# Kernel tuning notes

Measured on AMD Instinct MI355X. Metric: run time of the kernel, lower is better.

## Reference

```python
import jax, jax.numpy as jnp
import numpy as np

B, G, GS = 1024, 2000, 25   # batch, num gene groups, group size
H1, H2, C = 1024, 512, 10
EPS = 1e-5


def _xavier(key, shape, fan_in, fan_out):
    lim = np.sqrt(6.0 / (fan_in + fan_out))
    return jax.random.uniform(key, shape, jnp.float32, -lim, lim)


def setup_inputs() -> dict:
    key = jax.random.key(0)
    ks = jax.random.split(key, 8)
    x = jax.random.normal(ks[0], (B, G * GS), jnp.float32)
    # per-group Linear(GS, 1) weights stacked -> block-diagonal grouped GEMM
    gene_w = _xavier(ks[1], (G, GS), GS, 1)
    gene_b = jnp.zeros((G,), jnp.float32)
    W1 = _xavier(ks[2], (G, H1), G, H1)
    b1 = jnp.zeros((H1,), jnp.float32)
    W2 = _xavier(ks[3], (H1, H2), H1, H2)
    b2 = jnp.zeros((H2,), jnp.float32)
    Wout = _xavier(ks[4], (H2, C), H2, C)
    bout = jnp.zeros((C,), jnp.float32)
    Wres = _xavier(ks[5], (G, C), G, C)
    bres = jnp.zeros((C,), jnp.float32)
    gamma1 = jnp.ones((H1,), jnp.float32); beta1 = jnp.zeros((H1,), jnp.float32)
    gamma2 = jnp.ones((H2,), jnp.float32); beta2 = jnp.zeros((H2,), jnp.float32)
    return dict(x=x, gene_w=gene_w, gene_b=gene_b, W1=W1, b1=b1,
                gamma1=gamma1, beta1=beta1, W2=W2, b2=b2,
                gamma2=gamma2, beta2=beta2, Wout=Wout, bout=bout,
                Wres=Wres, bres=bres)


def _batch_norm(h, gamma, beta):
    # training-mode BatchNorm1d: biased batch statistics over axis 0
    mu = jnp.mean(h, axis=0)
    var = jnp.mean(jnp.square(h - mu), axis=0)
    return gamma * (h - mu) * jax.lax.rsqrt(var + EPS) + beta


def reference(x, gene_w, gene_b, W1, b1, gamma1, beta1, W2, b2,
              gamma2, beta2, Wout, bout, Wres, bres):
    # fused replacement for the per-group Linear(GS,1)+ReLU loop + cat
    xg = x.reshape(B, G, GS)
    g = jax.nn.relu(jnp.einsum('bgk,gk->bg', xg, gene_w) + gene_b)  # [B, G]
    h1 = jax.nn.relu(_batch_norm(g @ W1 + b1, gamma1, beta1))       # [B, H1]
    h2 = jax.nn.relu(_batch_norm(h1 @ W2 + b2, gamma2, beta2))      # [B, H2]
    x_main = h2 @ Wout + bout                                       # [B, C]
    x_res = g @ Wres + bres                                         # [B, C]
    return jax.nn.softmax(x_main + x_res, axis=1)
```

## Files before the change

### kernel.cpp

```cpp
#include <hip/hip_runtime.h>
#include <math.h>

#define NB   1024
#define NG   2000
#define NGS  25
#define KP   2048
#define NH1  1024
#define NH1X 1088
#define NH2  512
#define NC   10
#define EPSV 1e-5f
#define GPB  200
#define RB   8


typedef __attribute__((ext_vector_type(8)))  __bf16 bf16x8;
typedef __attribute__((ext_vector_type(4)))  float  f32x4;
typedef __attribute__((ext_vector_type(16))) float  f32x16;
typedef __attribute__((ext_vector_type(8)))  unsigned short u16x8;

__device__ __forceinline__ unsigned short f2bf(float f) {
  union { float f; unsigned u; } v; v.f = f;
  return (unsigned short)((v.u + 0x7fffu + ((v.u >> 16) & 1u)) >> 16);
}

__global__ __launch_bounds__(256) void prep_kernel(
    const float* __restrict__ x, const float* __restrict__ gw,
    const float* __restrict__ gb, unsigned short* __restrict__ g_bf,
    const float* __restrict__ W1, unsigned short* __restrict__ W1bT,
    const float* __restrict__ W2, unsigned short* __restrict__ W2bT,
    const float* __restrict__ Wres, float* __restrict__ stats) {
  __shared__ __attribute__((aligned(16))) float xs[2][GPB * NGS];
  int t = threadIdx.x;

  if (blockIdx.y < 10) {
    int blk = blockIdx.y;
    int b0 = blockIdx.x * RB;
    const size_t chunk_off = (size_t)blk * (GPB * NGS);

    float4 st[5];
#pragma unroll
    for (int j = 0; j < 5; ++j) st[j] = make_float4(0.f, 0.f, 0.f, 0.f);
    {
      const float4* s0 = (const float4*)(x + (size_t)b0 * (NG * NGS) + chunk_off);
#pragma unroll
      for (int j = 0; j < 5; ++j) {
        int i = t + j * 256;
        if (i < (GPB * NGS) / 4) st[j] = s0[i];
      }
    }
    const float4* gsrc = (const float4*)(gw + chunk_off);
    float4* xd0 = (float4*)xs[0];
    for (int i = t; i < (GPB * NGS) / 4; i += 256) xd0[i] = gsrc[i];
    __syncthreads();
    float gwr[NGS];
    float gbv = 0.f;
    int gi = blk * GPB + t;
    if (t < GPB) {
#pragma unroll
      for (int k = 0; k < NGS; ++k) gwr[k] = xs[0][t * NGS + k];
      gbv = gb[gi];
    }
    __syncthreads();

    for (int r = 0; r < RB; ++r) {
      float* xc = xs[r & 1];
      float4* xdc = (float4*)xc;
#pragma unroll
      for (int j = 0; j < 5; ++j) {
        int i = t + j * 256;
        if (i < (GPB * NGS) / 4) xdc[i] = st[j];
      }
      __syncthreads();
      if (r + 1 < RB) {
        const float4* sn = (const float4*)
            (x + (size_t)(b0 + r + 1) * (NG * NGS) + chunk_off);
#pragma unroll
        for (int j = 0; j < 5; ++j) {
          int i = t + j * 256;
          if (i < (GPB * NGS) / 4) st[j] = sn[i];
        }
      }
      int b = b0 + r;
      if (t < GPB) {
        float acc = 0.f;
        const float* xp = xc + t * NGS;
#pragma unroll
        for (int k = 0; k < NGS; ++k) acc = fmaf(xp[k], gwr[k], acc);
        g_bf[(size_t)b * KP + gi] = f2bf(fmaxf(acc + gbv, 0.f));
      } else if (blk == 9 && t < GPB + (KP - NG)) {
        g_bf[(size_t)b * KP + NG + (t - GPB)] = 0;
      }
    }
    return;
  }

  int px = (blockIdx.y - 10) * 128 + blockIdx.x;
  if (px == 672) {
    for (int i = t; i < 3072; i += 256) stats[i] = 0.f;
    return;
  }
  if (px > 672) return;
  const float* src; unsigned short* dst; int K, N, Kpad, k0, n0;
  int wres_mode = 0;
  if (px < 512)      { src = W1; dst = W1bT; K = NG;  N = NH1; Kpad = KP;
                       k0 = (px & 31) * 64; n0 = (px >> 5) * 64; }
  else if (px < 640) { int xi = px - 512;
                       src = W2; dst = W2bT; K = NH1; N = NH2; Kpad = NH1;
                       k0 = (xi & 15) * 64; n0 = (xi >> 4) * 64; }
  else               { int xi = px - 640;
                       src = Wres; dst = W1bT; K = NG; N = NC; Kpad = KP;
                       k0 = xi * 64; n0 = 1024; wres_mode = 1; }

  unsigned short (*ts)[72] = (unsigned short (*)[72])xs;
  int c4 = (t & 15) * 4;
  int r  = t >> 4;
  for (int rr = r; rr < 64; rr += 16) {
    int k = k0 + rr;
    float v[4] = {0.f, 0.f, 0.f, 0.f};
    if (!wres_mode) {
      if (k < K) {
        float4 q = *(const float4*)&src[(size_t)k * N + n0 + c4];
        v[0] = q.x; v[1] = q.y; v[2] = q.z; v[3] = q.w;
      }
    } else {
      if (k < K) {
#pragma unroll
        for (int i = 0; i < 4; ++i)
          if (c4 + i < NC) v[i] = src[(size_t)k * NC + c4 + i];
      }
    }
    ts[rr][c4 + 0] = f2bf(v[0]); ts[rr][c4 + 1] = f2bf(v[1]);
    ts[rr][c4 + 2] = f2bf(v[2]); ts[rr][c4 + 3] = f2bf(v[3]);
  }
  __syncthreads();
  int rr8 = (t & 7) * 8;
  int cc  = t >> 3;
  for (int c = cc; c < 64; c += 32) {
    u16x8 val;
#pragma unroll
    for (int i = 0; i < 8; ++i) val[i] = ts[rr8 + i][c];
    *(u16x8*)&dst[(size_t)(n0 + c) * Kpad + k0 + rr8] = val;
  }
}

__global__ __launch_bounds__(256) void gemm1_kernel(
    const unsigned short* __restrict__ A,
    const unsigned short* __restrict__ Bt,
    float* __restrict__ C, float* __restrict__ sum, float* __restrict__ sq,
    float* __restrict__ rpx, int M, int N, int Kp) {
  __shared__ unsigned short As[32][68];
  __shared__ unsigned short Bs[64][68];
  __shared__ float ebuf[2 * 64 * 17];
  int t = threadIdx.x;
  int m0 = blockIdx.y * 32, n0 = blockIdx.x * 64;
  int wave = t >> 6, lane = t & 63;
  int h = wave & 1;
  int p = wave >> 1;
  int l31 = lane & 31, l5 = lane >> 5;
  int srow = t >> 3, skc = (t & 7) * 8;

  f32x16 acc;
#pragma unroll
  for (int q = 0; q < 16; ++q) acc[q] = 0.f;

  const unsigned short* Ap = A + (size_t)(m0 + srow) * Kp + skc;
  const unsigned short* Bp = Bt + (size_t)(n0 + srow) * Kp + skc;
  size_t rstep = 32 * (size_t)Kp;

  u16x8 pa0 = *(const u16x8*)(Ap);
  u16x8 pb0 = *(const u16x8*)(Bp);
  u16x8 pb1 = *(const u16x8*)(Bp + rstep);

  for (int k0 = 0; k0 < Kp; k0 += 64) {
    *(u16x8*)&As[srow][skc]      = pa0;
    *(u16x8*)&Bs[srow][skc]      = pb0;
    *(u16x8*)&Bs[srow + 32][skc] = pb1;
    __syncthreads();
    if (k0 + 64 < Kp) {
      pa0 = *(const u16x8*)(Ap + k0 + 64);
      pb0 = *(const u16x8*)(Bp + k0 + 64);
      pb1 = *(const u16x8*)(Bp + k0 + 64 + rstep);
    }
    int kb = p * 32 + l5 * 8;
    {
      bf16x8 av = *(const bf16x8*)&As[l31][kb];
      bf16x8 bv = *(const bf16x8*)&Bs[h * 32 + l31][kb];
      acc = __builtin_amdgcn_mfma_f32_32x32x16_bf16(av, bv, acc, 0, 0, 0);
    }
    {
      bf16x8 av = *(const bf16x8*)&As[l31][kb + 16];
      bf16x8 bv = *(const bf16x8*)&Bs[h * 32 + l31][kb + 16];
      acc = __builtin_amdgcn_mfma_f32_32x32x16_bf16(av, bv, acc, 0, 0, 0);
    }
    __syncthreads();
  }

  float* eb = ebuf + (size_t)(h * 64 + lane) * 17;
  if (p == 1) {
#pragma unroll
    for (int r = 0; r < 16; ++r) eb[r] = acc[r];
  }
  __syncthreads();
  if (p == 0) {
    float s = 0.f, ss = 0.f;
#pragma unroll
    for (int r = 0; r < 16; ++r) {
      float v = acc[r] + eb[r];
      int row = m0 + (r & 3) + 8 * (r >> 2) + 4 * l5;
      if (n0 < N) {
        C[(size_t)row * N + n0 + h * 32 + l31] = v;
        s += v;
        ss = fmaf(v, v, ss);
      } else {
        rpx[(size_t)row * 64 + h * 32 + l31] = v;
      }
    }
    if (n0 < N) {
      s  += __shfl_down(s, 32, 64);
      ss += __shfl_down(ss, 32, 64);
      if (lane < 32) {
        atomicAdd(&sum[n0 + h * 32 + lane], s);
        atomicAdd(&sq[n0 + h * 32 + lane], ss);
      }
    }
  }
}

__global__ __launch_bounds__(256) void gemm2_kernel(
    const float* __restrict__ A,
    const unsigned short* __restrict__ Bt,
    float* __restrict__ C, const float* __restrict__ sum1,
    const float* __restrict__ sq1, const float* __restrict__ gam1,
    const float* __restrict__ bet1, float* __restrict__ sum2,
    float* __restrict__ sq2, int M, int N, int Kp) {
  __shared__ unsigned short As[32][72];
  __shared__ unsigned short Bs[32][72];
  __shared__ float sc1s[NH1], sh1s[NH1];
  int t = threadIdx.x;
  int m0 = blockIdx.y * 32, n0 = blockIdx.x * 32;
  int wave = t >> 6, lane = t & 63;
  int wm = (wave >> 1) * 16, wn = (wave & 1) * 16;
  int fm = lane & 15, fk = (lane >> 4) * 8;
  int srow = t >> 3, skc = (t & 7) * 8;

  for (int k = t; k < Kp; k += 256) {
    float mu  = sum1[k] * (1.f / NB);
    float var = sq1[k] * (1.f / NB) - mu * mu;
    float scv = gam1[k] * rsqrtf(var + EPSV);
    sc1s[k] = scv;
    sh1s[k] = fmaf(-mu, scv, bet1[k]);
  }

  f32x4 acc = (f32x4){0.f, 0.f, 0.f, 0.f};

  const float* Ap = A + (size_t)(m0 + srow) * Kp + skc;
  const unsigned short* Bp = Bt + (size_t)(n0 + srow) * Kp + skc;

  f32x4 pa0 = *(const f32x4*)(Ap);
  f32x4 pa1 = *(const f32x4*)(Ap + 4);
  u16x8 pb0 = *(const u16x8*)(Bp);
  __syncthreads();

  for (int k0 = 0; k0 < Kp; k0 += 64) {
    f32x4 scl = *(const f32x4*)&sc1s[k0 + skc];
    f32x4 sch = *(const f32x4*)&sc1s[k0 + skc + 4];
    f32x4 shl = *(const f32x4*)&sh1s[k0 + skc];
    f32x4 shh = *(const f32x4*)&sh1s[k0 + skc + 4];
    u16x8 a0;
#pragma unroll
    for (int i = 0; i < 4; ++i) {
      a0[i]     = f2bf(fmaxf(fmaf(pa0[i], scl[i], shl[i]), 0.f));
      a0[i + 4] = f2bf(fmaxf(fmaf(pa1[i], sch[i], shh[i]), 0.f));
    }
    *(u16x8*)&As[srow][skc] = a0;
    *(u16x8*)&Bs[srow][skc] = pb0;
    __syncthreads();
    if (k0 + 64 < Kp) {
      pa0 = *(const f32x4*)(Ap + k0 + 64);
      pa1 = *(const f32x4*)(Ap + k0 + 64 + 4);
      pb0 = *(const u16x8*)(Bp + k0 + 64);
    }
#pragma unroll
    for (int s = 0; s < 2; ++s) {
      bf16x8 af = *(const bf16x8*)&As[wm + fm][s * 32 + fk];
      bf16x8 bf = *(const bf16x8*)&Bs[wn + fm][s * 32 + fk];
      acc = __builtin_amdgcn_mfma_f32_16x16x32_bf16(af, bf, acc, 0, 0, 0);
    }
    __syncthreads();
  }

  int crow = (lane >> 4) * 4, ccol = lane & 15;
  float s = 0.f, ss = 0.f;
#pragma unroll
  for (int r = 0; r < 4; ++r) {
    float v = acc[r];
    int m = m0 + wm + crow + r;
    int n = n0 + wn + ccol;
    C[(size_t)m * N + n] = v;
    s += v;
    ss = fmaf(v, v, ss);
  }
  s  += __shfl_down(s, 32, 64);  s  += __shfl_down(s, 16, 64);
  ss += __shfl_down(ss, 32, 64); ss += __shfl_down(ss, 16, 64);
  if (lane < 16) {
    atomicAdd(&sum2[n0 + wn + lane], s);
    atomicAdd(&sq2[n0 + wn + lane], ss);
  }
}

__global__ __launch_bounds__(256) void final_kernel(
    const float* __restrict__ t2, const float* __restrict__ sum2,
    const float* __restrict__ sq2, const float* __restrict__ gam2,
    const float* __restrict__ bet2, const float* __restrict__ rpx,
    const float* __restrict__ Wout, const float* __restrict__ bout,
    const float* __restrict__ bres, float* __restrict__ out) {
  __shared__ __attribute__((aligned(16))) float wl[NH2 * NC];
  __shared__ float red[4][NC];
  __shared__ float logits[NC];
  int b = blockIdx.x;
  int t = threadIdx.x;

  const float4* wsrc = (const float4*)Wout;
  float4* wdst = (float4*)wl;
#pragma unroll
  for (int i = 0; i < (NH2 * NC / 4) / 256; ++i)
    wdst[t + i * 256] = wsrc[t + i * 256];
  __syncthreads();

  float acc[NC] = {};
#pragma unroll
  for (int half = 0; half < 2; ++half) {
    int h = t + half * 256;
    float raw = t2[(size_t)b * NH2 + h];
    float mu  = sum2[h] * (1.f / NB);
    float var = sq2[h] * (1.f / NB) - mu * mu;
    float scv = gam2[h] * rsqrtf(var + EPSV);
    float hr  = fmaxf(fmaf(raw, scv, fmaf(-mu, scv, bet2[h])), 0.f);
    const float* wrow = &wl[h * NC];
#pragma unroll
    for (int c = 0; c < NC; ++c) acc[c] = fmaf(hr, wrow[c], acc[c]);
  }

  int lane = t & 63, wave = t >> 6;
#pragma unroll
  for (int c = 0; c < NC; ++c) {
    float v = acc[c];
    for (int off = 32; off > 0; off >>= 1) v += __shfl_down(v, off, 64);
    if (lane == 0) red[wave][c] = v;
  }
  __syncthreads();
  if (t < NC) {
    logits[t] = red[0][t] + red[1][t] + red[2][t] + red[3][t] +
                bout[t] + bres[t] + rpx[(size_t)b * 64 + t];
  }
  __syncthreads();
  if (t == 0) {
    float mx = logits[0];
#pragma unroll
    for (int c = 1; c < NC; ++c) mx = fmaxf(mx, logits[c]);
    float e[NC], s = 0.f;
#pragma unroll
    for (int c = 0; c < NC; ++c) { e[c] = expf(logits[c] - mx); s += e[c]; }
    float inv = 1.f / s;
#pragma unroll
    for (int c = 0; c < NC; ++c) out[(size_t)b * NC + c] = e[c] * inv;
  }
}

extern "C" void kernel_launch(void* const* d_in, const int* in_sizes, int n_in,
                              void* d_out, int out_size, void* d_ws, size_t ws_size,
                              hipStream_t stream) {
  const float* x      = (const float*)d_in[0];
  const float* gw     = (const float*)d_in[1];
  const float* gb     = (const float*)d_in[2];
  const float* W1     = (const float*)d_in[3];
  const float* gamma1 = (const float*)d_in[5];
  const float* beta1  = (const float*)d_in[6];
  const float* W2     = (const float*)d_in[7];
  const float* gamma2 = (const float*)d_in[9];
  const float* beta2  = (const float*)d_in[10];
  const float* Wout   = (const float*)d_in[11];
  const float* bout   = (const float*)d_in[12];
  const float* Wres   = (const float*)d_in[13];
  const float* bres   = (const float*)d_in[14];
  float* out = (float*)d_out;

  char* p = (char*)d_ws;
  unsigned short* g_bf = (unsigned short*)p; p += (size_t)NB * KP * 2;
  unsigned short* W1bT = (unsigned short*)p; p += (size_t)NH1X * KP * 2;
  unsigned short* W2bT = (unsigned short*)p; p += (size_t)NH2 * NH1 * 2;
  float* t1 = (float*)p; p += (size_t)NB * NH1 * 4;
  float* t2 = (float*)p; p += (size_t)NB * NH2 * 4;
  float* stats = (float*)p; p += 3072 * 4;
  float* rpx = (float*)p; p += (size_t)NB * 64 * 4;
  float* sum1 = stats, *sq1 = stats + 1024, *sum2 = stats + 2048, *sq2 = stats + 2560;

  prep_kernel<<<dim3(128, 16), 256, 0, stream>>>(x, gw, gb, g_bf,
                                                 W1, W1bT, W2, W2bT,
                                                 Wres, stats);

  gemm1_kernel<<<dim3(NH1X / 64, NB / 32), 256, 0, stream>>>(
      g_bf, W1bT, t1, sum1, sq1, rpx, NB, NH1, KP);

  gemm2_kernel<<<dim3(NH2 / 32, NB / 32), 256, 0, stream>>>(
      t1, W2bT, t2, sum1, sq1, gamma1, beta1, sum2, sq2, NB, NH2, NH1);

  final_kernel<<<NB, 256, 0, stream>>>(t2, sum2, sq2, gamma2, beta2, rpx,
                                       Wout, bout, bres, out);
}
```

Baseline: 359.8 us.

## Split gene-dot prep into per-wave smem slices to drop block barriers

Restructures the grouped gene dot-product stage so each of the four waves owns a 50-group slice of the 200-group chunk in its own shared-memory region. Each wave loads its slice with a 2-float alignment offset. Because no wave reads another wave's data, the __syncthreads barriers inside the row loop go away. The loop also double-buffers row loads in registers (stA/stB) so the next row's global load overlaps the current dot product. In exchange it uses more registers and relies on wave-synchronous ordering of LDS writes and reads within a wave.

Result: no change. 355.5 us (-1.2%).

```diff
diff --git a/kernel.cpp b/kernel.cpp
--- a/kernel.cpp
+++ b/kernel.cpp
@@ -30,67 +30,86 @@
     const float* __restrict__ W1, unsigned short* __restrict__ W1bT,
     const float* __restrict__ W2, unsigned short* __restrict__ W2bT,
     const float* __restrict__ Wres, float* __restrict__ stats) {
-  __shared__ __attribute__((aligned(16))) float xs[2][GPB * NGS];
+  __shared__ __attribute__((aligned(16))) float xsl[4][1284];
   int t = threadIdx.x;
 
   if (blockIdx.y < 10) {
     int blk = blockIdx.y;
     int b0 = blockIdx.x * RB;
-    const size_t chunk_off = (size_t)blk * (GPB * NGS);
-
-    float4 st[5];
-#pragma unroll
-    for (int j = 0; j < 5; ++j) st[j] = make_float4(0.f, 0.f, 0.f, 0.f);
+    int w = t >> 6, l = t & 63;
+    int d = (w & 1) * 2;
+    size_t wchunk = (size_t)blk * (GPB * NGS) + w * 1250 - d;
+    float4* slice4 = (float4*)xsl[w];
+    const float* xrd = xsl[w] + d;
+
+    float4 sg[5], stA[5], stB[5];
+    const float4* gw4 = (const float4*)gw + (wchunk >> 2);
+#pragma unroll
+    for (int j = 0; j < 5; ++j) {
+      int idx = l + j * 64;
+      sg[j] = (idx < 313) ? gw4[idx] : make_float4(0.f, 0.f, 0.f, 0.f);
+    }
     {
-      const float4* s0 = (const float4*)(x + (size_t)b0 * (NG * NGS) + chunk_off);
+      const float4* x0 = (const float4*)x + (((size_t)b0 * (NG * NGS) + wchunk) >> 2);
 #pragma unroll
       for (int j = 0; j < 5; ++j) {
-        int i = t + j * 256;
-        if (i < (GPB * NGS) / 4) st[j] = s0[i];
-      }
-    }
-    const float4* gsrc = (const float4*)(gw + chunk_off);
-    float4* xd0 = (float4*)xs[0];
-    for (int i = t; i < (GPB * NGS) / 4; i += 256) xd0[i] = gsrc[i];
-    __syncthreads();
+        int idx = l + j * 64;
+        stA[j] = (idx < 313) ? x0[idx] : make_float4(0.f, 0.f, 0.f, 0.f);
+      }
+    }
+#pragma unroll
+    for (int j = 0; j < 5; ++j) {
+      int idx = l + j * 64;
+      if (idx < 313) slice4[idx] = sg[j];
+    }
     float gwr[NGS];
     float gbv = 0.f;
-    int gi = blk * GPB + t;
-    if (t < GPB) {
-#pragma unroll
-      for (int k = 0; k < NGS; ++k) gwr[k] = xs[0][t * NGS + k];
-      gbv = gb[gi];
-    }
-    __syncthreads();
-
-    for (int r = 0; r < RB; ++r) {
-      float* xc = xs[r & 1];
-      float4* xdc = (float4*)xc;
+    if (l < 50) {
+#pragma unroll
+      for (int k = 0; k < NGS; ++k) gwr[k] = xrd[l * 25 + k];
+      gbv = gb[blk * GPB + w * 50 + l];
+    }
+
+    auto publish = [&](const float4* st) {
 #pragma unroll
       for (int j = 0; j < 5; ++j) {
-        int i = t + j * 256;
-        if (i < (GPB * NGS) / 4) xdc[i] = st[j];
-      }
-      __syncthreads();
-      if (r + 1 < RB) {
-        const float4* sn = (const float4*)
-            (x + (size_t)(b0 + r + 1) * (NG * NGS) + chunk_off);
-#pragma unroll
-        for (int j = 0; j < 5; ++j) {
-          int i = t + j * 256;
-          if (i < (GPB * NGS) / 4) st[j] = sn[i];
+        int idx = l + j * 64;
+        if (idx < 313) slice4[idx] = st[j];
+      }
+    };
+    auto issue = [&](float4* st, int row) {
+      const float4* xn = (const float4*)x + (((size_t)row * (NG * NGS) + wchunk) >> 2);
+#pragma unroll
+      for (int j = 0; j < 5; ++j) {
+        int idx = l + j * 64;
+        st[j] = (idx < 313) ? xn[idx] : make_float4(0.f, 0.f, 0.f, 0.f);
+      }
+    };
+    auto dot = [&](int b) {
+      if (l < 50) {
+        float acc = 0.f;
+#pragma unroll
+        for (int k = 0; k < NGS; ++k) acc = fmaf(xrd[l * 25 + k], gwr[k], acc);
+        g_bf[(size_t)b * KP + blk * GPB + w * 50 + l] =
+            f2bf(fmaxf(acc + gbv, 0.f));
+      } else if (blk == 9 && w == 0) {
+#pragma unroll
+        for (int j = 0; j < 4; ++j) {
+          int pp = (l - 50) + 14 * j;
+          if (pp < KP - NG) g_bf[(size_t)b * KP + NG + pp] = 0;
         }
       }
-      int b = b0 + r;
-      if (t < GPB) {
-        float acc = 0.f;
-        const float* xp = xc + t * NGS;
-#pragma unroll
-        for (int k = 0; k < NGS; ++k) acc = fmaf(xp[k], gwr[k], acc);
-        g_bf[(size_t)b * KP + gi] = f2bf(fmaxf(acc + gbv, 0.f));
-      } else if (blk == 9 && t < GPB + (KP - NG)) {
-        g_bf[(size_t)b * KP + NG + (t - GPB)] = 0;
-      }
+    };
+
+#pragma unroll
+    for (int rr = 0; rr < RB / 2; ++rr) {
+      int rA = rr * 2;
+      publish(stA);
+      issue(stB, b0 + rA + 1);
+      dot(b0 + rA);
+      publish(stB);
+      if (rA + 2 < RB) issue(stA, b0 + rA + 2);
+      dot(b0 + rA + 1);
     }
     return;
   }
@@ -112,7 +131,7 @@
                        src = Wres; dst = W1bT; K = NG; N = NC; Kpad = KP;
                        k0 = xi * 64; n0 = 1024; wres_mode = 1; }
 
-  unsigned short (*ts)[72] = (unsigned short (*)[72])xs;
+  unsigned short (*ts)[72] = (unsigned short (*)[72])xsl;
   int c4 = (t & 15) * 4;
   int r  = t >> 4;
   for (int rr = r; rr < 64; rr += 16) {
```

## Compute grouped gene projection with block-diagonal bf16 MFMA GEMM tiles

Applied to the files above, without the earlier changes.

Replaces the scalar per-group dot-product stage with a tiled MFMA formulation. Each block takes 32 batch rows and 64 groups and builds a block-diagonal bf16 weight tile in shared memory. It streams x converted to bf16 and accumulates with 32x32x16 MFMA, with a split-K reduction across wave pairs. The aim is to make the memory-bound x read more efficient through wider, better-distributed tiles and a larger grid. In exchange it wastes most MFMA work on zeros and rounds x to bf16 before the reduction, which lowers accuracy.

Result: no change. 362.4 us (+0.7%).

```diff
diff --git a/kernel.cpp b/kernel.cpp
--- a/kernel.cpp
+++ b/kernel.cpp
@@ -4,14 +4,13 @@
 #define NB   1024
 #define NG   2000
 #define NGS  25
+#define XW   (NG * NGS)
 #define KP   2048
 #define NH1  1024
 #define NH1X 1088
 #define NH2  512
 #define NC   10
 #define EPSV 1e-5f
-#define GPB  200
-#define RB   8
 
 
 typedef __attribute__((ext_vector_type(8)))  __bf16 bf16x8;
@@ -30,72 +29,99 @@
     const float* __restrict__ W1, unsigned short* __restrict__ W1bT,
     const float* __restrict__ W2, unsigned short* __restrict__ W2bT,
     const float* __restrict__ Wres, float* __restrict__ stats) {
-  __shared__ __attribute__((aligned(16))) float xs[2][GPB * NGS];
+  __shared__ __attribute__((aligned(16))) char smem[34816];
   int t = threadIdx.x;
 
-  if (blockIdx.y < 10) {
-    int blk = blockIdx.y;
-    int b0 = blockIdx.x * RB;
-    const size_t chunk_off = (size_t)blk * (GPB * NGS);
-
-    float4 st[5];
-#pragma unroll
-    for (int j = 0; j < 5; ++j) st[j] = make_float4(0.f, 0.f, 0.f, 0.f);
+  if (blockIdx.y < 32) {
+    unsigned short (*As)[68] = (unsigned short (*)[68])smem;
+    unsigned short (*Bs)[68] = (unsigned short (*)[68])(smem + 8704);
+    float* ebuf = (float*)(smem + 8704 + 17408);
+    int g0 = blockIdx.x * 64;
+    int m0 = blockIdx.y * 32;
+    int wave = t >> 6, lane = t & 63;
+    int h = wave & 1, p = wave >> 1;
+    int l31 = lane & 31, l5 = lane >> 5;
+    int srow = t >> 3, skc = (t & 7) * 8;
+
+    f32x16 acc;
+#pragma unroll
+    for (int q = 0; q < 16; ++q) acc[q] = 0.f;
+
+    const float* xrow = x + (size_t)(m0 + srow) * XW;
+    const int cbase = g0 * NGS + skc;
+    const float* gwb = gw + (size_t)g0 * NGS;
+
+    float4 pa0 = make_float4(0.f, 0.f, 0.f, 0.f), pa1 = pa0;
     {
-      const float4* s0 = (const float4*)(x + (size_t)b0 * (NG * NGS) + chunk_off);
-#pragma unroll
-      for (int j = 0; j < 5; ++j) {
-        int i = t + j * 256;
-        if (i < (GPB * NGS) / 4) st[j] = s0[i];
-      }
-    }
-    const float4* gsrc = (const float4*)(gw + chunk_off);
-    float4* xd0 = (float4*)xs[0];
-    for (int i = t; i < (GPB * NGS) / 4; i += 256) xd0[i] = gsrc[i];
+      int c0 = cbase;
+      if (c0 + 4 <= XW) pa0 = *(const float4*)(xrow + c0);
+      if (c0 + 8 <= XW) pa1 = *(const float4*)(xrow + c0 + 4);
+    }
+    {
+      u16x8 z = (u16x8){0, 0, 0, 0, 0, 0, 0, 0};
+      unsigned short* bflat = &Bs[0][0];
+      *(u16x8*)(bflat + (size_t)t * 8) = z;
+      *(u16x8*)(bflat + (size_t)(t + 256) * 8) = z;
+      if (t < 32) *(u16x8*)(bflat + (size_t)(t + 512) * 8) = z;
+    }
+
+    for (int k0 = 0; k0 < 1600; k0 += 64) {
+      u16x8 a;
+      a[0] = f2bf(pa0.x); a[1] = f2bf(pa0.y); a[2] = f2bf(pa0.z); a[3] = f2bf(pa0.w);
+      a[4] = f2bf(pa1.x); a[5] = f2bf(pa1.y); a[6] = f2bf(pa1.z); a[7] = f2bf(pa1.w);
+      *(u16x8*)&As[srow][skc] = a;
+      if (t < 64) {
+        int kk = k0 + t;
+        if (k0 > 0) {
+          int no = ((kk - 64) * 5243) >> 17;
+          Bs[no][t] = 0;
+        }
+        int nn = (kk * 5243) >> 17;
+        int gcol = g0 * NGS + kk;
+        Bs[nn][t] = (gcol < XW) ? f2bf(gwb[kk]) : (unsigned short)0;
+      }
+      __syncthreads();
+      if (k0 + 64 < 1600) {
+        int c0 = cbase + k0 + 64;
+        pa0 = (c0 + 4 <= XW) ? *(const float4*)(xrow + c0)
+                             : make_float4(0.f, 0.f, 0.f, 0.f);
+        pa1 = (c0 + 8 <= XW) ? *(const float4*)(xrow + c0 + 4)
+                             : make_float4(0.f, 0.f, 0.f, 0.f);
+      }
+      int kb = p * 32 + l5 * 8;
+      {
+        bf16x8 av = *(const bf16x8*)&As[l31][kb];
+        bf16x8 bv = *(const bf16x8*)&Bs[h * 32 + l31][kb];
+        acc = __builtin_amdgcn_mfma_f32_32x32x16_bf16(av, bv, acc, 0, 0, 0);
+      }
+      {
+        bf16x8 av = *(const bf16x8*)&As[l31][kb + 16];
+        bf16x8 bv = *(const bf16x8*)&Bs[h * 32 + l31][kb + 16];
+        acc = __builtin_amdgcn_mfma_f32_32x32x16_bf16(av, bv, acc, 0, 0, 0);
+      }
+      __syncthreads();
+    }
+
+    float* eb = ebuf + (size_t)(h * 64 + lane) * 17;
+    if (p == 1) {
+#pragma unroll
+      for (int r = 0; r < 16; ++r) eb[r] = acc[r];
+    }
     __syncthreads();
-    float gwr[NGS];
-    float gbv = 0.f;
-    int gi = blk * GPB + t;
-    if (t < GPB) {
-#pragma unroll
-      for (int k = 0; k < NGS; ++k) gwr[k] = xs[0][t * NGS + k];
-      gbv = gb[gi];
-    }
-    __syncthreads();
-
-    for (int r = 0; r < RB; ++r) {
-      float* xc = xs[r & 1];
-      float4* xdc = (float4*)xc;
-#pragma unroll
-      for (int j = 0; j < 5; ++j) {
-        int i = t + j * 256;
-        if (i < (GPB * NGS) / 4) xdc[i] = st[j];
-      }
-      __syncthreads();
-      if (r + 1 < RB) {
-        const float4* sn = (const float4*)
-            (x + (size_t)(b0 + r + 1) * (NG * NGS) + chunk_off);
-#pragma unroll
-        for (int j = 0; j < 5; ++j) {
-          int i = t + j * 256;
-          if (i < (GPB * NGS) / 4) st[j] = sn[i];
-        }
-      }
-      int b = b0 + r;
-      if (t < GPB) {
-        float acc = 0.f;
-        const float* xp = xc + t * NGS;
-#pragma unroll
-        for (int k = 0; k < NGS; ++k) acc = fmaf(xp[k], gwr[k], acc);
-        g_bf[(size_t)b * KP + gi] = f2bf(fmaxf(acc + gbv, 0.f));
-      } else if (blk == 9 && t < GPB + (KP - NG)) {
-        g_bf[(size_t)b * KP + NG + (t - GPB)] = 0;
+    if (p == 0) {
+#pragma unroll
+      for (int r = 0; r < 16; ++r) {
+        float v = acc[r] + eb[r];
+        int row = m0 + (r & 3) + 8 * (r >> 2) + 4 * l5;
+        int col = g0 + h * 32 + l31;
+        float bias = (col < NG) ? gb[col] : 0.f;
+        g_bf[(size_t)row * KP + col] = f2bf(fmaxf(v + bias, 0.f));
       }
     }
     return;
   }
 
-  int px = (blockIdx.y - 10) * 128 + blockIdx.x;
+  int px = (blockIdx.y - 32) * 32 + blockIdx.x;
   if (px == 672) {
     for (int i = t; i < 3072; i += 256) stats[i] = 0.f;
     return;
@@ -112,7 +138,7 @@
                        src = Wres; dst = W1bT; K = NG; N = NC; Kpad = KP;
                        k0 = xi * 64; n0 = 1024; wres_mode = 1; }
 
-  unsigned short (*ts)[72] = (unsigned short (*)[72])xs;
+  unsigned short (*ts)[72] = (unsigned short (*)[72])smem;
   int c4 = (t & 15) * 4;
   int r  = t >> 4;
   for (int rr = r; rr < 64; rr += 16) {
@@ -396,9 +422,9 @@
   float* rpx = (float*)p; p += (size_t)NB * 64 * 4;
   float* sum1 = stats, *sq1 = stats + 1024, *sum2 = stats + 2048, *sq2 = stats + 2560;
 
-  prep_kernel<<<dim3(128, 16), 256, 0, stream>>>(x, gw, gb, g_bf,
-                                                 W1, W1bT, W2, W2bT,
-                                                 Wres, stats);
+  prep_kernel<<<dim3(32, 54), 256, 0, stream>>>(x, gw, gb, g_bf,
+                                                W1, W1bT, W2, W2bT,
+                                                Wres, stats);
 
   gemm1_kernel<<<dim3(NH1X / 64, NB / 32), 256, 0, stream>>>(
       g_bf, W1bT, t1, sum1, sq1, rpx, NB, NH1, KP);
```

## Read x directly from global into registers for gene-group dot products

Applied to the files above, without the earlier changes.

The gene-group reduction stage of prep_kernel no longer stages x rows through double-buffered shared memory. Each lane now loads 100 contiguous floats (4 groups) straight from global memory into registers and multiplies them against transposed gene weights held in registers. Each block covers 256 groups across 8 rows, and each lane writes 4 bf16 outputs at once, including the zero padding. This removes the LDS round trip and barriers, but per-lane strided 400-byte reads may coalesce worse and register pressure rises with 25 f32x4 weight registers.

New measurement: 372.4 us. 3.5% more time.

```diff
diff --git a/kernel.cpp b/kernel.cpp
--- a/kernel.cpp
+++ b/kernel.cpp
@@ -4,20 +4,20 @@
 #define NB   1024
 #define NG   2000
 #define NGS  25
+#define XW   (NG * NGS)
 #define KP   2048
 #define NH1  1024
 #define NH1X 1088
 #define NH2  512
 #define NC   10
 #define EPSV 1e-5f
-#define GPB  200
-#define RB   8
 
 
 typedef __attribute__((ext_vector_type(8)))  __bf16 bf16x8;
 typedef __attribute__((ext_vector_type(4)))  float  f32x4;
 typedef __attribute__((ext_vector_type(16))) float  f32x16;
 typedef __attribute__((ext_vector_type(8)))  unsigned short u16x8;
+typedef __attribute__((ext_vector_type(4)))  unsigned short u16x4;
 
 __device__ __forceinline__ unsigned short f2bf(float f) {
   union { float f; unsigned u; } v; v.f = f;
@@ -30,72 +30,71 @@
     const float* __restrict__ W1, unsigned short* __restrict__ W1bT,
     const float* __restrict__ W2, unsigned short* __restrict__ W2bT,
     const float* __restrict__ Wres, float* __restrict__ stats) {
-  __shared__ __attribute__((aligned(16))) float xs[2][GPB * NGS];
+  __shared__ __attribute__((aligned(16))) char smem[26624];
   int t = threadIdx.x;
 
-  if (blockIdx.y < 10) {
-    int blk = blockIdx.y;
-    int b0 = blockIdx.x * RB;
-    const size_t chunk_off = (size_t)blk * (GPB * NGS);
-
-    float4 st[5];
-#pragma unroll
-    for (int j = 0; j < 5; ++j) st[j] = make_float4(0.f, 0.f, 0.f, 0.f);
-    {
-      const float4* s0 = (const float4*)(x + (size_t)b0 * (NG * NGS) + chunk_off);
-#pragma unroll
-      for (int j = 0; j < 5; ++j) {
-        int i = t + j * 256;
-        if (i < (GPB * NGS) / 4) st[j] = s0[i];
-      }
-    }
-    const float4* gsrc = (const float4*)(gw + chunk_off);
-    float4* xd0 = (float4*)xs[0];
-    for (int i = t; i < (GPB * NGS) / 4; i += 256) xd0[i] = gsrc[i];
+  if (blockIdx.y < 8) {
+    float (*wT)[256] = (float (*)[256])smem;
+    int G0 = blockIdx.y * 256;
+    int r0 = blockIdx.x * 8;
+    int w = t >> 6, l = t & 63;
+
+    int fmax = (NG - G0 < 256 ? NG - G0 : 256) * NGS;
+    const float* gwb = gw + (size_t)G0 * NGS;
+    for (int i = t; i < 256 * NGS; i += 256) {
+      float v = (i < fmax) ? gwb[i] : 0.f;
+      wT[i % NGS][i / NGS] = v;
+    }
     __syncthreads();
-    float gwr[NGS];
-    float gbv = 0.f;
-    int gi = blk * GPB + t;
-    if (t < GPB) {
-#pragma unroll
-      for (int k = 0; k < NGS; ++k) gwr[k] = xs[0][t * NGS + k];
-      gbv = gb[gi];
-    }
-    __syncthreads();
-
-    for (int r = 0; r < RB; ++r) {
-      float* xc = xs[r & 1];
-      float4* xdc = (float4*)xc;
-#pragma unroll
-      for (int j = 0; j < 5; ++j) {
-        int i = t + j * 256;
-        if (i < (GPB * NGS) / 4) xdc[i] = st[j];
-      }
-      __syncthreads();
-      if (r + 1 < RB) {
-        const float4* sn = (const float4*)
-            (x + (size_t)(b0 + r + 1) * (NG * NGS) + chunk_off);
-#pragma unroll
-        for (int j = 0; j < 5; ++j) {
-          int i = t + j * 256;
-          if (i < (GPB * NGS) / 4) st[j] = sn[i];
+
+    bool act = (4 * l) < (NG - G0);
+    f32x4 wreg[25];
+#pragma unroll
+    for (int k = 0; k < NGS; ++k) wreg[k] = *(const f32x4*)&wT[k][4 * l];
+    f32x4 gb4 = (f32x4){0.f, 0.f, 0.f, 0.f};
+    if (act) gb4 = *(const f32x4*)&gb[G0 + 4 * l];
+
+    const size_t colb = (size_t)G0 * NGS + (size_t)l * 100;
+    for (int rr = 0; rr < 2; ++rr) {
+      int r = r0 + w * 2 + rr;
+      const float4* xp = (const float4*)(x + (size_t)r * XW + colb);
+      float acc[4] = {0.f, 0.f, 0.f, 0.f};
+      if (act) {
+        float4 xa[13];
+#pragma unroll
+        for (int j = 0; j < 13; ++j) xa[j] = xp[j];
+#pragma unroll
+        for (int j = 0; j < 13; ++j) {
+          float e[4] = {xa[j].x, xa[j].y, xa[j].z, xa[j].w};
+#pragma unroll
+          for (int i = 0; i < 4; ++i) {
+            int f = 4 * j + i;
+            acc[f / 25] = fmaf(e[i], wreg[f % 25][f / 25], acc[f / 25]);
+          }
+        }
+        float4 xb[12];
+#pragma unroll
+        for (int j = 0; j < 12; ++j) xb[j] = xp[13 + j];
+#pragma unroll
+        for (int j = 0; j < 12; ++j) {
+          float e[4] = {xb[j].x, xb[j].y, xb[j].z, xb[j].w};
+#pragma unroll
+          for (int i = 0; i < 4; ++i) {
+            int f = 4 * (13 + j) + i;
+            acc[f / 25] = fmaf(e[i], wreg[f % 25][f / 25], acc[f / 25]);
+          }
         }
       }
-      int b = b0 + r;
-      if (t < GPB) {
-        float acc = 0.f;
-        const float* xp = xc + t * NGS;
-#pragma unroll
-        for (int k = 0; k < NGS; ++k) acc = fmaf(xp[k], gwr[k], acc);
-        g_bf[(size_t)b * KP + gi] = f2bf(fmaxf(acc + gbv, 0.f));
-      } else if (blk == 9 && t < GPB + (KP - NG)) {
-        g_bf[(size_t)b * KP + NG + (t - GPB)] = 0;
-      }
+      u16x4 o;
+#pragma unroll
+      for (int q = 0; q < 4; ++q)
+        o[q] = act ? f2bf(fmaxf(acc[q] + gb4[q], 0.f)) : (unsigned short)0;
+      *(u16x4*)&g_bf[(size_t)r * KP + G0 + 4 * l] = o;
     }
     return;
   }
 
-  int px = (blockIdx.y - 10) * 128 + blockIdx.x;
+  int px = (blockIdx.y - 8) * 128 + blockIdx.x;
   if (px == 672) {
     for (int i = t; i < 3072; i += 256) stats[i] = 0.f;
     return;
@@ -112,7 +111,7 @@
                        src = Wres; dst = W1bT; K = NG; N = NC; Kpad = KP;
                        k0 = xi * 64; n0 = 1024; wres_mode = 1; }
 
-  unsigned short (*ts)[72] = (unsigned short (*)[72])xs;
+  unsigned short (*ts)[72] = (unsigned short (*)[72])smem;
   int c4 = (t & 15) * 4;
   int r  = t >> 4;
   for (int rr = r; rr < 64; rr += 16) {
@@ -396,7 +395,7 @@
   float* rpx = (float*)p; p += (size_t)NB * 64 * 4;
   float* sum1 = stats, *sq1 = stats + 1024, *sum2 = stats + 2048, *sq2 = stats + 2560;
 
-  prep_kernel<<<dim3(128, 16), 256, 0, stream>>>(x, gw, gb, g_bf,
+  prep_kernel<<<dim3(128, 14), 256, 0, stream>>>(x, gw, gb, g_bf,
                                                  W1, W1bT, W2, W2bT,
                                                  Wres, stats);
 
```
